# Optimization experiments

Measured on AMD Instinct MI355X. Metric: run time of the kernel, lower is better.

## Reference

```python
import jax, jax.numpy as jnp
import numpy as np

B, S, D, H = 4, 2048, 512, 8

def setup_inputs() -> dict:
    key = jax.random.key(0)
    ks = jax.random.split(key, 6)
    query = jax.random.normal(ks[0], (B, S, D), dtype=jnp.float32)
    value = jax.random.normal(ks[1], (B, S, D), dtype=jnp.float32)
    # causal additive mask, broadcast over heads: [H, S, S]
    causal = jnp.where(jnp.tril(jnp.ones((S, S), dtype=bool)), 0.0, -1e9).astype(jnp.float32)
    mask = jnp.broadcast_to(causal[None, :, :], (H, S, S))
    sd = 1.0 / np.sqrt(D)
    Wq = jax.random.normal(ks[2], (D, D), dtype=jnp.float32) * sd
    Wkv = jax.random.normal(ks[3], (D, 2 * D), dtype=jnp.float32) * sd
    Wo = jax.random.normal(ks[4], (D, D), dtype=jnp.float32) * sd
    normalizer = jnp.asarray(1.0 / np.sqrt(D // H), dtype=jnp.float32)  # 1/sqrt(head_size)
    head_mults = jnp.ones((1, 1, H, 1), dtype=jnp.float32)
    return {"query": query, "value": value, "mask": mask, "Wq": Wq, "Wkv": Wkv,
            "Wo": Wo, "normalizer": normalizer, "head_mults": head_mults}

def reference(query, value, mask, Wq, Wkv, Wo, normalizer, head_mults):
    b, sq, d = query.shape
    h = head_mults.shape[2]
    q = (query @ Wq).reshape(b, sq, h, -1)                 # [b,q,h,hd]
    k, v = jnp.split(value @ Wkv, 2, axis=-1)
    sk = value.shape[1]
    k = k.reshape(b, sk, h, -1)
    v = v.reshape(b, sk, h, -1)
    score = jnp.einsum('bqhd,bkhd->bhqk', q, k) * normalizer
    score = score + mask[None, :, :, :]
    align = jax.nn.softmax(score, axis=-1)
    heads = jnp.einsum('bhqk,bkhd->bqhd', align, v)        # [b,q,h,hd]
    # cross-head normalization (over head axis, ddof=0 like tf.reduce_std)
    mean = jnp.mean(heads, axis=-2, keepdims=True)
    std = jnp.std(heads, axis=-2, keepdims=True)
    heads = (heads - mean) / (std + 0.01)
    heads = heads * head_mults
    out = heads.reshape(b, sq, d) @ Wo
    return out
```

## Files before the change

### kernel.cpp

```cpp
#include <hip/hip_runtime.h>


typedef float  f32x4  __attribute__((ext_vector_type(4)));
typedef __bf16 bf16x8 __attribute__((ext_vector_type(8)));
typedef short  s16x4  __attribute__((ext_vector_type(4)));
typedef unsigned short u16;

#define BS 2048
#define DD 512
#define NH 8

__device__ __forceinline__ u16 f2bf(float f) {
  union { float f; unsigned u; } v; v.f = f;
  unsigned r = v.u + 0x7fffu + ((v.u >> 16) & 1u);
  return (u16)(r >> 16);
}
__device__ __forceinline__ float bf2f(u16 b) {
  union { unsigned u; float f; } v; v.u = ((unsigned)b) << 16; return v.f;
}
__device__ __forceinline__ u16 cvt1(float f) {
  __bf16 h = (__bf16)f;
  return __builtin_bit_cast(u16, h);
}

__device__ __forceinline__ void gll16(const u16* g, u16* l) {
  __builtin_amdgcn_global_load_lds((const __attribute__((address_space(1))) void*)g,
                                   (__attribute__((address_space(3))) void*)l, 16, 0, 0);
}

__global__ __launch_bounds__(256) void prep(const float* __restrict__ Wq,
                                            const float* __restrict__ Wkv,
                                            const float* __restrict__ Wo,
                                            u16* __restrict__ WqT, u16* __restrict__ WkvT,
                                            u16* __restrict__ WoT) {
  __shared__ float Ts[64][65];
  const int t = threadIdx.x;
  int tb = blockIdx.x;
  const float* W; u16* Wt; int N, ntn;
  if (tb < 64)       { W = Wq;  Wt = WqT;  N = 512;  ntn = 8; }
  else if (tb < 192) { W = Wkv; Wt = WkvT; N = 1024; ntn = 16; tb -= 64; }
  else               { W = Wo;  Wt = WoT;  N = 512;  ntn = 8;  tb -= 192; }
  int tk = tb / ntn, tn = tb - tk * ntn;
  int r = t >> 2, c0 = (t & 3) * 16;
  const float* src = &W[(long)(tk * 64 + r) * N + tn * 64 + c0];
#pragma unroll
  for (int j = 0; j < 4; ++j) {
    float4 x = *(const float4*)(src + j * 4);
    Ts[r][c0 + j * 4 + 0] = x.x; Ts[r][c0 + j * 4 + 1] = x.y;
    Ts[r][c0 + j * 4 + 2] = x.z; Ts[r][c0 + j * 4 + 3] = x.w;
  }
  __syncthreads();
  u16* dst = &Wt[(long)(tn * 64 + r) * 512 + tk * 64 + c0];
#pragma unroll
  for (int m = 0; m < 4; ++m) {
    ushort4 o;
    o.x = f2bf(Ts[c0 + m * 4 + 0][r]); o.y = f2bf(Ts[c0 + m * 4 + 1][r]);
    o.z = f2bf(Ts[c0 + m * 4 + 2][r]); o.w = f2bf(Ts[c0 + m * 4 + 3][r]);
    *(ushort4*)(dst + m * 4) = o;
  }
}

template <int AF32>
__device__ __forceinline__ void gemm_core64(const void* __restrict__ Av,
                                            const u16* __restrict__ Bt,
                                            int m0, int n0, int K,
                                            u16* Al, u16* Bl, f32x4 acc[4][4]) {
  const int t = threadIdx.x;
  const int wv = t >> 6, ln = t & 63, qd = ln >> 4, l16 = ln & 15;
  const int rw = (wv & 1) * 64, cw = (wv >> 1) * 64;
  const int srB = wv * 16 + (ln >> 2), scB = (ln & 3) * 8;
  const int srA = t >> 1, scA = (t & 1) * 16;
  for (int k0 = 0; k0 < K; k0 += 64) {
    __syncthreads();
    if (AF32) {
      const float* Af = (const float*)Av;
#pragma unroll
      for (int p = 0; p < 2; ++p) {
        const float* src = &Af[(long)(m0 + srA) * K + k0 + p * 32 + scA];
        float4 x0 = *(const float4*)src;
        float4 x1 = *(const float4*)(src + 4);
        float4 x2 = *(const float4*)(src + 8);
        float4 x3 = *(const float4*)(src + 12);
        bf16x8 o0, o1;
        o0[0] = (__bf16)x0.x; o0[1] = (__bf16)x0.y; o0[2] = (__bf16)x0.z; o0[3] = (__bf16)x0.w;
        o0[4] = (__bf16)x1.x; o0[5] = (__bf16)x1.y; o0[6] = (__bf16)x1.z; o0[7] = (__bf16)x1.w;
        o1[0] = (__bf16)x2.x; o1[1] = (__bf16)x2.y; o1[2] = (__bf16)x2.z; o1[3] = (__bf16)x2.w;
        o1[4] = (__bf16)x3.x; o1[5] = (__bf16)x3.y; o1[6] = (__bf16)x3.z; o1[7] = (__bf16)x3.w;
        u16* dst = &Al[p * 4096 + srA * 32 + scA];
        *(bf16x8*)dst = o0;
        *(bf16x8*)(dst + 8) = o1;
      }
    } else {
      const u16* Ab = (const u16*)Av;
#pragma unroll
      for (int p = 0; p < 2; ++p)
#pragma unroll
        for (int c = 0; c < 2; ++c) {
          int r = c * 64 + srB;
          gll16(&Ab[(long)(m0 + r) * K + k0 + p * 32 + scB], &Al[p * 4096 + r * 32 + scB]);
        }
    }
#pragma unroll
    for (int p = 0; p < 2; ++p)
#pragma unroll
      for (int c = 0; c < 2; ++c) {
        int r = c * 64 + srB;
        gll16(&Bt[(long)(n0 + r) * K + k0 + p * 32 + scB], &Bl[p * 4096 + r * 32 + scB]);
      }
    __syncthreads();
#pragma unroll
    for (int p = 0; p < 2; ++p) {
      bf16x8 af[4], bfr[4];
#pragma unroll
      for (int i = 0; i < 4; ++i)
        af[i] = *(const bf16x8*)&Al[p * 4096 + (rw + i * 16 + l16) * 32 + qd * 8];
#pragma unroll
      for (int j = 0; j < 4; ++j)
        bfr[j] = *(const bf16x8*)&Bl[p * 4096 + (cw + j * 16 + l16) * 32 + qd * 8];
#pragma unroll
      for (int i = 0; i < 4; ++i)
#pragma unroll
        for (int j = 0; j < 4; ++j)
          acc[i][j] = __builtin_amdgcn_mfma_f32_16x16x32_bf16(af[i], bfr[j], acc[i][j], 0, 0, 0);
    }
  }
}

__global__ __launch_bounds__(256) void qkv_gemm(const float* __restrict__ query,
                                                const float* __restrict__ value,
                                                const u16* __restrict__ WqT,
                                                const u16* __restrict__ WkvT,
                                                u16* __restrict__ Qb,
                                                u16* __restrict__ Kb,
                                                u16* __restrict__ Vt) {
  __shared__ __align__(16) u16 Al[2 * 128 * 32];
  __shared__ __align__(16) u16 Bl[2 * 128 * 32];
  const bool isQ = blockIdx.y < 4;
  const void* A = isQ ? (const void*)query : (const void*)value;
  const u16* Bt = isQ ? WqT : WkvT;
  const int n0 = (isQ ? blockIdx.y : blockIdx.y - 4) * 128;
  const int m0 = blockIdx.x * 128;
  f32x4 acc[4][4] = {};
  gemm_core64<1>(A, Bt, m0, n0, 512, Al, Bl, acc);
  const int t = threadIdx.x;
  const int wv = t >> 6, ln = t & 63, qd = ln >> 4, l16 = ln & 15;
  const int rw = (wv & 1) * 64, cw = (wv >> 1) * 64;
  if (isQ) {
#pragma unroll
    for (int i = 0; i < 4; ++i)
#pragma unroll
      for (int j = 0; j < 4; ++j) {
        int row = m0 + rw + i * 16 + qd * 4, col = n0 + cw + j * 16 + l16;
#pragma unroll
        for (int r = 0; r < 4; ++r)
          Qb[(long)(row + r) * 512 + col] = cvt1(acc[i][j][r]);
      }
  } else {
#pragma unroll
    for (int j = 0; j < 4; ++j) {
      int col = n0 + cw + j * 16 + l16;
      if (col < 512) {
#pragma unroll
        for (int i = 0; i < 4; ++i) {
          int row = m0 + rw + i * 16 + qd * 4;
#pragma unroll
          for (int r = 0; r < 4; ++r)
            Kb[(long)(row + r) * 512 + col] = cvt1(acc[i][j][r]);
        }
      } else {
        int c2 = col - 512, hh = c2 >> 6, dd = c2 & 63;
#pragma unroll
        for (int i = 0; i < 4; ++i) {
          int sg = m0 + rw + i * 16 + qd * 4;
          int bb = sg >> 11, ss = sg & 2047;
          ushort4 o;
          o.x = cvt1(acc[i][j][0]); o.y = cvt1(acc[i][j][1]);
          o.z = cvt1(acc[i][j][2]); o.w = cvt1(acc[i][j][3]);
          *(ushort4*)&Vt[((long)(bb * 8 + hh) * 64 + dd) * 2048 + ss] = o;
        }
      }
    }
  }
}

__global__ __launch_bounds__(256) void out_gemm(const u16* __restrict__ A,
                                                const u16* __restrict__ Bt,
                                                float* __restrict__ C) {
  __shared__ __align__(16) u16 Al[2 * 128 * 32];
  __shared__ __align__(16) u16 Bl[2 * 128 * 32];
  const int m0 = blockIdx.x * 128, n0 = blockIdx.y * 128;
  f32x4 acc[4][4] = {};
  gemm_core64<0>(A, Bt, m0, n0, 512, Al, Bl, acc);
  const int t = threadIdx.x;
  const int wv = t >> 6, ln = t & 63, qd = ln >> 4, l16 = ln & 15;
  const int rw = (wv & 1) * 64, cw = (wv >> 1) * 64;
#pragma unroll
  for (int i = 0; i < 4; ++i)
#pragma unroll
    for (int j = 0; j < 4; ++j) {
      int row = m0 + rw + i * 16 + qd * 4, col = n0 + cw + j * 16 + l16;
#pragma unroll
      for (int r = 0; r < 4; ++r)
        C[(long)(row + r) * 512 + col] = acc[i][j][r];
    }
}

__device__ __forceinline__ void attn_phase(const u16* ks, const u16* vs,
                                           const bf16x8 bq[2], f32x4 o[4],
                                           float& l_i, float scale2, bool diag,
                                           int wv, int qd, int l16) {
  constexpr int ST = 72;
  f32x4 s[4] = {};
#pragma unroll
  for (int c = 0; c < 2; ++c)
#pragma unroll
    for (int nt = 0; nt < 4; ++nt) {
      bf16x8 ak = *(const bf16x8*)&ks[(nt * 16 + l16) * ST + c * 32 + qd * 8];
      s[nt] = __builtin_amdgcn_mfma_f32_16x16x32_bf16(ak, bq[c], s[nt], 0, 0, 0);
    }
  if (diag) {
    const int limi = wv * 16 + l16;
#pragma unroll
    for (int nt = 0; nt < 4; ++nt)
#pragma unroll
      for (int r = 0; r < 4; ++r) {
        float v = s[nt][r] * scale2;
        if (nt * 16 + qd * 4 + r > limi) v = -INFINITY;
        float p = exp2f(v);
        s[nt][r] = p;
        l_i += p;
      }
  } else {
#pragma unroll
    for (int nt = 0; nt < 4; ++nt)
#pragma unroll
      for (int r = 0; r < 4; ++r) {
        float p = exp2f(s[nt][r] * scale2);
        s[nt][r] = p;
        l_i += p;
      }
  }
#pragma unroll
  for (int cp = 0; cp < 2; ++cp) {
    bf16x8 pb;
#pragma unroll
    for (int j = 0; j < 4; ++j) {
      pb[j] = (__bf16)s[cp * 2][j];
      pb[4 + j] = (__bf16)s[cp * 2 + 1][j];
    }
#pragma unroll
    for (int n2 = 0; n2 < 4; ++n2) {
      bf16x8 av;
      s16x4* ah = (s16x4*)&av;
      const u16* vp = &vs[(n2 * 16 + l16) * ST + cp * 32 + qd * 4];
      ah[0] = *(const s16x4*)vp;
      ah[1] = *(const s16x4*)(vp + 16);
      o[n2] = __builtin_amdgcn_mfma_f32_16x16x32_bf16(av, pb, o[n2], 0, 0, 0);
    }
  }
}

__global__ __launch_bounds__(256, 2) void attn(const u16* __restrict__ Qb,
                                               const u16* __restrict__ Kb,
                                               const u16* __restrict__ Vt,
                                               u16* __restrict__ heads,
                                               const float* __restrict__ normp) {
  constexpr int ST = 72;
  __shared__ __align__(16) u16 Ks[2][64 * ST];
  __shared__ __align__(16) u16 Vts[2][64 * ST];
  const float scale2 = normp[0] * 1.44269504f;
  const int t = threadIdx.x;
  const int wv = t >> 6, ln = t & 63, qd = ln >> 4, l16 = ln & 15;
  const int sr = t >> 2, scg = (t & 3) * 16;
  const int bid = blockIdx.x;
  const int hb = (bid & 7) + 8 * (bid >> 7);
  const int qtS = (bid >> 3) & 15, qtL = 31 - qtS;
  const int h = hb & 7, b = hb >> 3;
  const int bs0 = b * BS;
  const u16* vtb = Vt + ((long)(b * 8 + h) * 64) * 2048;

  bf16x8 bqS[2], bqL[2];
#pragma unroll
  for (int c = 0; c < 2; ++c) {
    bqS[c] = *(const bf16x8*)&Qb[(long)(bs0 + qtS * 64 + wv * 16 + l16) * 512 + h * 64 + c * 32 + qd * 8];
    bqL[c] = *(const bf16x8*)&Qb[(long)(bs0 + qtL * 64 + wv * 16 + l16) * 512 + h * 64 + c * 32 + qd * 8];
  }

  bf16x8 kr0, kr1, vr0, vr1;
#define FETCH(KB) do { \
    const u16* kp_ = &Kb[(long)(bs0 + (KB) * 64 + sr) * 512 + h * 64 + scg]; \
    kr0 = *(const bf16x8*)kp_; kr1 = *(const bf16x8*)(kp_ + 8); \
    const u16* vp_ = &vtb[(long)sr * 2048 + (KB) * 64 + scg]; \
    vr0 = *(const bf16x8*)vp_; vr1 = *(const bf16x8*)(vp_ + 8); } while (0)
  FETCH(0);
  float lS = 0.f, lL = 0.f;
  f32x4 oS[4] = {}, oL[4] = {};

  for (int kb = 0; kb <= qtL; ++kb) {
    const int buf = kb & 1;
    *(bf16x8*)&Ks[buf][sr * ST + scg] = kr0;
    *(bf16x8*)&Ks[buf][sr * ST + scg + 8] = kr1;
    *(bf16x8*)&Vts[buf][sr * ST + scg] = vr0;
    *(bf16x8*)&Vts[buf][sr * ST + scg + 8] = vr1;
    __syncthreads();
    if (kb < qtL) FETCH(kb + 1);

    attn_phase(Ks[buf], Vts[buf], bqL, oL, lL, scale2, kb == qtL, wv, qd, l16);
    if (kb <= qtS)
      attn_phase(Ks[buf], Vts[buf], bqS, oS, lS, scale2, kb == qtS, wv, qd, l16);
  }
#undef FETCH

  lL += __shfl_xor(lL, 16); lL += __shfl_xor(lL, 32);
  lS += __shfl_xor(lS, 16); lS += __shfl_xor(lS, 32);
  float invL = 1.f / lL, invS = 1.f / lS;
  __syncthreads();
#pragma unroll
  for (int n2 = 0; n2 < 4; ++n2)
#pragma unroll
    for (int r = 0; r < 4; ++r) {
      Ks[0][(wv * 16 + l16) * ST + n2 * 16 + qd * 4 + r] = cvt1(oL[n2][r] * invL);
      Vts[0][(wv * 16 + l16) * ST + n2 * 16 + qd * 4 + r] = cvt1(oS[n2][r] * invS);
    }
  __syncthreads();
  {
    u16* dstL = &heads[(long)(bs0 + qtL * 64 + sr) * 512 + h * 64 + scg];
    *(bf16x8*)dstL = *(const bf16x8*)&Ks[0][sr * ST + scg];
    *(bf16x8*)(dstL + 8) = *(const bf16x8*)&Ks[0][sr * ST + scg + 8];
    u16* dstS = &heads[(long)(bs0 + qtS * 64 + sr) * 512 + h * 64 + scg];
    *(bf16x8*)dstS = *(const bf16x8*)&Vts[0][sr * ST + scg];
    *(bf16x8*)(dstS + 8) = *(const bf16x8*)&Vts[0][sr * ST + scg + 8];
  }
}

__global__ __launch_bounds__(256) void headnorm(const u16* __restrict__ heads,
                                                const float* __restrict__ hm,
                                                u16* __restrict__ outn) {
  int i = blockIdx.x * 256 + threadIdx.x;
  int d = i & 63, bs = i >> 6;
  const u16* p = heads + (long)bs * DD + d;
  float x[NH], mean = 0.f;
#pragma unroll
  for (int h = 0; h < NH; ++h) { x[h] = bf2f(p[h * 64]); mean += x[h]; }
  mean *= 0.125f;
  float var = 0.f;
#pragma unroll
  for (int h = 0; h < NH; ++h) { float dd = x[h] - mean; var += dd * dd; }
  var *= 0.125f;
  float inv = 1.f / (sqrtf(var) + 0.01f);
#pragma unroll
  for (int h = 0; h < NH; ++h)
    outn[(long)bs * DD + h * 64 + d] = cvt1((x[h] - mean) * inv * hm[h]);
}

extern "C" void kernel_launch(void* const* d_in, const int* in_sizes, int n_in,
                              void* d_out, int out_size, void* d_ws, size_t ws_size,
                              hipStream_t stream) {
  const float* query = (const float*)d_in[0];
  const float* value = (const float*)d_in[1];
  const float* Wq    = (const float*)d_in[3];
  const float* Wkv   = (const float*)d_in[4];
  const float* Wo    = (const float*)d_in[5];
  const float* normp = (const float*)d_in[6];
  const float* hmult = (const float*)d_in[7];

  char* ws = (char*)d_ws;
  const size_t MB = 1 << 20;
  u16*   WqT   = (u16*)(ws);
  u16*   WkvT  = (u16*)(ws + 524288);
  u16*   WoT   = (u16*)(ws + 1 * MB + 524288);
  u16*   Qb    = (u16*)(ws + 2 * MB);
  u16*   Kb    = (u16*)(ws + 10 * MB);
  u16*   Vt    = (u16*)(ws + 18 * MB);
  u16*   heads = (u16*)(ws + 26 * MB);
  u16*   hN    = (u16*)(ws + 34 * MB);

  prep<<<256, 256, 0, stream>>>(Wq, Wkv, Wo, WqT, WkvT, WoT);
  qkv_gemm<<<dim3(64, 12), 256, 0, stream>>>(query, value, WqT, WkvT, Qb, Kb, Vt);
  attn<<<512, 256, 0, stream>>>(Qb, Kb, Vt, heads, normp);
  headnorm<<<(4 * BS * 64) / 256, 256, 0, stream>>>(heads, hmult, hN);
  out_gemm<<<dim3(64, 4), 256, 0, stream>>>(hN, WoT, (float*)d_out);
}
```

Before: 281.3 us.

## Fuse all five stages into one cooperative persistent kernel with grid syncs

```diff
diff --git a/kernel.cpp b/kernel.cpp
--- a/kernel.cpp
+++ b/kernel.cpp
@@ -1,5 +1,8 @@
 #include <hip/hip_runtime.h>
-
+#include <hip/hip_cooperative_groups.h>
+
+
+namespace cg = cooperative_groups;
 
 typedef float  f32x4  __attribute__((ext_vector_type(4)));
 typedef __bf16 bf16x8 __attribute__((ext_vector_type(8)));
@@ -28,14 +31,13 @@
                                    (__attribute__((address_space(3))) void*)l, 16, 0, 0);
 }
 
-__global__ __launch_bounds__(256) void prep(const float* __restrict__ Wq,
-                                            const float* __restrict__ Wkv,
-                                            const float* __restrict__ Wo,
-                                            u16* __restrict__ WqT, u16* __restrict__ WkvT,
-                                            u16* __restrict__ WoT) {
-  __shared__ float Ts[64][65];
-  const int t = threadIdx.x;
-  int tb = blockIdx.x;
+
+__device__ __forceinline__ void prep_body(int tb, int t,
+                                          const float* __restrict__ Wq,
+                                          const float* __restrict__ Wkv,
+                                          const float* __restrict__ Wo,
+                                          u16* __restrict__ WqT, u16* __restrict__ WkvT,
+                                          u16* __restrict__ WoT, float (*Ts)[65]) {
   const float* W; u16* Wt; int N, ntn;
   if (tb < 64)       { W = Wq;  Wt = WqT;  N = 512;  ntn = 8; }
   else if (tb < 192) { W = Wkv; Wt = WkvT; N = 1024; ntn = 16; tb -= 64; }
@@ -126,6 +128,289 @@
   }
 }
 
+__device__ __forceinline__ void qkv_tile(int bx, int by,
+                                         const float* __restrict__ query,
+                                         const float* __restrict__ value,
+                                         const u16* __restrict__ WqT,
+                                         const u16* __restrict__ WkvT,
+                                         u16* __restrict__ Qb, u16* __restrict__ Kb,
+                                         u16* __restrict__ Vt, u16* Al, u16* Bl) {
+  const bool isQ = by < 4;
+  const void* A = isQ ? (const void*)query : (const void*)value;
+  const u16* Bt = isQ ? WqT : WkvT;
+  const int n0 = (isQ ? by : by - 4) * 128;
+  const int m0 = bx * 128;
+  f32x4 acc[4][4] = {};
+  gemm_core64<1>(A, Bt, m0, n0, 512, Al, Bl, acc);
+  const int t = threadIdx.x;
+  const int wv = t >> 6, ln = t & 63, qd = ln >> 4, l16 = ln & 15;
+  const int rw = (wv & 1) * 64, cw = (wv >> 1) * 64;
+  if (isQ) {
+#pragma unroll
+    for (int i = 0; i < 4; ++i)
+#pragma unroll
+      for (int j = 0; j < 4; ++j) {
+        int row = m0 + rw + i * 16 + qd * 4, col = n0 + cw + j * 16 + l16;
+#pragma unroll
+        for (int r = 0; r < 4; ++r)
+          Qb[(long)(row + r) * 512 + col] = cvt1(acc[i][j][r]);
+      }
+  } else {
+#pragma unroll
+    for (int j = 0; j < 4; ++j) {
+      int col = n0 + cw + j * 16 + l16;
+      if (col < 512) {
+#pragma unroll
+        for (int i = 0; i < 4; ++i) {
+          int row = m0 + rw + i * 16 + qd * 4;
+#pragma unroll
+          for (int r = 0; r < 4; ++r)
+            Kb[(long)(row + r) * 512 + col] = cvt1(acc[i][j][r]);
+        }
+      } else {
+        int c2 = col - 512, hh = c2 >> 6, dd = c2 & 63;
+#pragma unroll
+        for (int i = 0; i < 4; ++i) {
+          int sg = m0 + rw + i * 16 + qd * 4;
+          int bb = sg >> 11, ss = sg & 2047;
+          ushort4 o;
+          o.x = cvt1(acc[i][j][0]); o.y = cvt1(acc[i][j][1]);
+          o.z = cvt1(acc[i][j][2]); o.w = cvt1(acc[i][j][3]);
+          *(ushort4*)&Vt[((long)(bb * 8 + hh) * 64 + dd) * 2048 + ss] = o;
+        }
+      }
+    }
+  }
+}
+
+__device__ __forceinline__ void out_tile(int bx, int by,
+                                         const u16* __restrict__ A,
+                                         const u16* __restrict__ Bt,
+                                         float* __restrict__ C, u16* Al, u16* Bl) {
+  const int m0 = bx * 128, n0 = by * 128;
+  f32x4 acc[4][4] = {};
+  gemm_core64<0>(A, Bt, m0, n0, 512, Al, Bl, acc);
+  const int t = threadIdx.x;
+  const int wv = t >> 6, ln = t & 63, qd = ln >> 4, l16 = ln & 15;
+  const int rw = (wv & 1) * 64, cw = (wv >> 1) * 64;
+#pragma unroll
+  for (int i = 0; i < 4; ++i)
+#pragma unroll
+    for (int j = 0; j < 4; ++j) {
+      int row = m0 + rw + i * 16 + qd * 4, col = n0 + cw + j * 16 + l16;
+#pragma unroll
+      for (int r = 0; r < 4; ++r)
+        C[(long)(row + r) * 512 + col] = acc[i][j][r];
+    }
+}
+
+__device__ __forceinline__ void attn_phase(const u16* ks, const u16* vs,
+                                           const bf16x8 bq[2], f32x4 o[4],
+                                           float& l_i, float scale2, bool diag,
+                                           int wv, int qd, int l16) {
+  constexpr int ST = 72;
+  f32x4 s[4] = {};
+#pragma unroll
+  for (int c = 0; c < 2; ++c)
+#pragma unroll
+    for (int nt = 0; nt < 4; ++nt) {
+      bf16x8 ak = *(const bf16x8*)&ks[(nt * 16 + l16) * ST + c * 32 + qd * 8];
+      s[nt] = __builtin_amdgcn_mfma_f32_16x16x32_bf16(ak, bq[c], s[nt], 0, 0, 0);
+    }
+  if (diag) {
+    const int limi = wv * 16 + l16;
+#pragma unroll
+    for (int nt = 0; nt < 4; ++nt)
+#pragma unroll
+      for (int r = 0; r < 4; ++r) {
+        float v = s[nt][r] * scale2;
+        if (nt * 16 + qd * 4 + r > limi) v = -INFINITY;
+        float p = exp2f(v);
+        s[nt][r] = p;
+        l_i += p;
+      }
+  } else {
+#pragma unroll
+    for (int nt = 0; nt < 4; ++nt)
+#pragma unroll
+      for (int r = 0; r < 4; ++r) {
+        float p = exp2f(s[nt][r] * scale2);
+        s[nt][r] = p;
+        l_i += p;
+      }
+  }
+#pragma unroll
+  for (int cp = 0; cp < 2; ++cp) {
+    bf16x8 pb;
+#pragma unroll
+    for (int j = 0; j < 4; ++j) {
+      pb[j] = (__bf16)s[cp * 2][j];
+      pb[4 + j] = (__bf16)s[cp * 2 + 1][j];
+    }
+#pragma unroll
+    for (int n2 = 0; n2 < 4; ++n2) {
+      bf16x8 av;
+      s16x4* ah = (s16x4*)&av;
+      const u16* vp = &vs[(n2 * 16 + l16) * ST + cp * 32 + qd * 4];
+      ah[0] = *(const s16x4*)vp;
+      ah[1] = *(const s16x4*)(vp + 16);
+      o[n2] = __builtin_amdgcn_mfma_f32_16x16x32_bf16(av, pb, o[n2], 0, 0, 0);
+    }
+  }
+}
+
+__device__ __forceinline__ void attn_block(int bid,
+                                           const u16* __restrict__ Qb,
+                                           const u16* __restrict__ Kb,
+                                           const u16* __restrict__ Vt,
+                                           u16* __restrict__ heads, float scale2,
+                                           u16* KsB, u16* VtsB) {
+  constexpr int ST = 72;
+  constexpr int BUF = 64 * ST;
+  const int t = threadIdx.x;
+  const int wv = t >> 6, ln = t & 63, qd = ln >> 4, l16 = ln & 15;
+  const int sr = t >> 2, scg = (t & 3) * 16;
+  const int hb = (bid & 7) + 8 * (bid >> 7);
+  const int qtS = (bid >> 3) & 15, qtL = 31 - qtS;
+  const int h = hb & 7, b = hb >> 3;
+  const int bs0 = b * BS;
+  const u16* vtb = Vt + ((long)(b * 8 + h) * 64) * 2048;
+
+  bf16x8 bqS[2], bqL[2];
+#pragma unroll
+  for (int c = 0; c < 2; ++c) {
+    bqS[c] = *(const bf16x8*)&Qb[(long)(bs0 + qtS * 64 + wv * 16 + l16) * 512 + h * 64 + c * 32 + qd * 8];
+    bqL[c] = *(const bf16x8*)&Qb[(long)(bs0 + qtL * 64 + wv * 16 + l16) * 512 + h * 64 + c * 32 + qd * 8];
+  }
+
+  bf16x8 kr0, kr1, vr0, vr1;
+#define FETCH(KB) do { \
+    const u16* kp_ = &Kb[(long)(bs0 + (KB) * 64 + sr) * 512 + h * 64 + scg]; \
+    kr0 = *(const bf16x8*)kp_; kr1 = *(const bf16x8*)(kp_ + 8); \
+    const u16* vp_ = &vtb[(long)sr * 2048 + (KB) * 64 + scg]; \
+    vr0 = *(const bf16x8*)vp_; vr1 = *(const bf16x8*)(vp_ + 8); } while (0)
+  FETCH(0);
+  float lS = 0.f, lL = 0.f;
+  f32x4 oS[4] = {}, oL[4] = {};
+
+  for (int kb = 0; kb <= qtL; ++kb) {
+    u16* Ksb = KsB + (kb & 1) * BUF;
+    u16* Vtsb = VtsB + (kb & 1) * BUF;
+    *(bf16x8*)&Ksb[sr * ST + scg] = kr0;
+    *(bf16x8*)&Ksb[sr * ST + scg + 8] = kr1;
+    *(bf16x8*)&Vtsb[sr * ST + scg] = vr0;
+    *(bf16x8*)&Vtsb[sr * ST + scg + 8] = vr1;
+    __syncthreads();
+    if (kb < qtL) FETCH(kb + 1);
+
+    attn_phase(Ksb, Vtsb, bqL, oL, lL, scale2, kb == qtL, wv, qd, l16);
+    if (kb <= qtS)
+      attn_phase(Ksb, Vtsb, bqS, oS, lS, scale2, kb == qtS, wv, qd, l16);
+  }
+#undef FETCH
+
+  lL += __shfl_xor(lL, 16); lL += __shfl_xor(lL, 32);
+  lS += __shfl_xor(lS, 16); lS += __shfl_xor(lS, 32);
+  float invL = 1.f / lL, invS = 1.f / lS;
+  __syncthreads();
+#pragma unroll
+  for (int n2 = 0; n2 < 4; ++n2)
+#pragma unroll
+    for (int r = 0; r < 4; ++r) {
+      KsB[(wv * 16 + l16) * ST + n2 * 16 + qd * 4 + r] = cvt1(oL[n2][r] * invL);
+      VtsB[(wv * 16 + l16) * ST + n2 * 16 + qd * 4 + r] = cvt1(oS[n2][r] * invS);
+    }
+  __syncthreads();
+  {
+    u16* dstL = &heads[(long)(bs0 + qtL * 64 + sr) * 512 + h * 64 + scg];
+    *(bf16x8*)dstL = *(const bf16x8*)&KsB[sr * ST + scg];
+    *(bf16x8*)(dstL + 8) = *(const bf16x8*)&KsB[sr * ST + scg + 8];
+    u16* dstS = &heads[(long)(bs0 + qtS * 64 + sr) * 512 + h * 64 + scg];
+    *(bf16x8*)dstS = *(const bf16x8*)&VtsB[sr * ST + scg];
+    *(bf16x8*)(dstS + 8) = *(const bf16x8*)&VtsB[sr * ST + scg + 8];
+  }
+}
+
+__device__ __forceinline__ void headnorm_i(int i, const u16* __restrict__ heads,
+                                           const float* __restrict__ hm,
+                                           u16* __restrict__ outn) {
+  int d = i & 63, bs = i >> 6;
+  const u16* p = heads + (long)bs * DD + d;
+  float x[NH], mean = 0.f;
+#pragma unroll
+  for (int h = 0; h < NH; ++h) { x[h] = bf2f(p[h * 64]); mean += x[h]; }
+  mean *= 0.125f;
+  float var = 0.f;
+#pragma unroll
+  for (int h = 0; h < NH; ++h) { float dd = x[h] - mean; var += dd * dd; }
+  var *= 0.125f;
+  float inv = 1.f / (sqrtf(var) + 0.01f);
+#pragma unroll
+  for (int h = 0; h < NH; ++h)
+    outn[(long)bs * DD + h * 64 + d] = cvt1((x[h] - mean) * inv * hm[h]);
+}
+
+__global__ __launch_bounds__(256, 2) void fused(const float* __restrict__ query,
+                                                const float* __restrict__ value,
+                                                const float* __restrict__ Wq,
+                                                const float* __restrict__ Wkv,
+                                                const float* __restrict__ Wo,
+                                                const float* __restrict__ normp,
+                                                const float* __restrict__ hmult,
+                                                u16* __restrict__ WqT,
+                                                u16* __restrict__ WkvT,
+                                                u16* __restrict__ WoT,
+                                                u16* __restrict__ Qb,
+                                                u16* __restrict__ Kb,
+                                                u16* __restrict__ Vt,
+                                                u16* __restrict__ heads,
+                                                u16* __restrict__ hN,
+                                                float* __restrict__ out) {
+  __shared__ __align__(16) unsigned char smraw[36864];
+  const int t = threadIdx.x;
+  const int bid = blockIdx.x;
+  cg::grid_group grid = cg::this_grid();
+  const float scale2 = normp[0] * 1.44269504f;
+
+  if (bid < 256)
+    prep_body(bid, t, Wq, Wkv, Wo, WqT, WkvT, WoT, (float(*)[65])smraw);
+  __threadfence();
+  grid.sync();
+
+  {
+    u16* Al = (u16*)smraw;
+    u16* Bl = (u16*)(smraw + 16384);
+    for (int tile = bid; tile < 768; tile += 512)
+      qkv_tile(tile & 63, tile >> 6, query, value, WqT, WkvT, Qb, Kb, Vt, Al, Bl);
+  }
+  __threadfence();
+  grid.sync();
+
+  attn_block(bid, Qb, Kb, Vt, heads, scale2, (u16*)smraw, (u16*)(smraw + 18432));
+  __threadfence();
+  grid.sync();
+
+  for (int i = bid * 256 + t; i < 4 * BS * 64; i += 512 * 256)
+    headnorm_i(i, heads, hmult, hN);
+  __threadfence();
+  grid.sync();
+
+  if (bid < 256) {
+    u16* Al = (u16*)smraw;
+    u16* Bl = (u16*)(smraw + 16384);
+    out_tile(bid & 63, bid >> 6, hN, WoT, out, Al, Bl);
+  }
+}
+
+__global__ __launch_bounds__(256) void prep(const float* __restrict__ Wq,
+                                            const float* __restrict__ Wkv,
+                                            const float* __restrict__ Wo,
+                                            u16* __restrict__ WqT, u16* __restrict__ WkvT,
+                                            u16* __restrict__ WoT) {
+  __shared__ float Ts[64][65];
+  prep_body(blockIdx.x, threadIdx.x, Wq, Wkv, Wo, WqT, WkvT, WoT, Ts);
+}
+
 __global__ __launch_bounds__(256) void qkv_gemm(const float* __restrict__ query,
                                                 const float* __restrict__ value,
                                                 const u16* __restrict__ WqT,
@@ -135,52 +420,23 @@
                                                 u16* __restrict__ Vt) {
   __shared__ __align__(16) u16 Al[2 * 128 * 32];
   __shared__ __align__(16) u16 Bl[2 * 128 * 32];
-  const bool isQ = blockIdx.y < 4;
-  const void* A = isQ ? (const void*)query : (const void*)value;
-  const u16* Bt = isQ ? WqT : WkvT;
-  const int n0 = (isQ ? blockIdx.y : blockIdx.y - 4) * 128;
-  const int m0 = blockIdx.x * 128;
-  f32x4 acc[4][4] = {};
-  gemm_core64<1>(A, Bt, m0, n0, 512, Al, Bl, acc);
-  const int t = threadIdx.x;
-  const int wv = t >> 6, ln = t & 63, qd = ln >> 4, l16 = ln & 15;
-  const int rw = (wv & 1) * 64, cw = (wv >> 1) * 64;
-  if (isQ) {
-#pragma unroll
-    for (int i = 0; i < 4; ++i)
-#pragma unroll
-      for (int j = 0; j < 4; ++j) {
-        int row = m0 + rw + i * 16 + qd * 4, col = n0 + cw + j * 16 + l16;
-#pragma unroll
-        for (int r = 0; r < 4; ++r)
-          Qb[(long)(row + r) * 512 + col] = cvt1(acc[i][j][r]);
-      }
-  } else {
-#pragma unroll
-    for (int j = 0; j < 4; ++j) {
-      int col = n0 + cw + j * 16 + l16;
-      if (col < 512) {
-#pragma unroll
-        for (int i = 0; i < 4; ++i) {
-          int row = m0 + rw + i * 16 + qd * 4;
-#pragma unroll
-          for (int r = 0; r < 4; ++r)
-            Kb[(long)(row + r) * 512 + col] = cvt1(acc[i][j][r]);
-        }
-      } else {
-        int c2 = col - 512, hh = c2 >> 6, dd = c2 & 63;
-#pragma unroll
-        for (int i = 0; i < 4; ++i) {
-          int sg = m0 + rw + i * 16 + qd * 4;
-          int bb = sg >> 11, ss = sg & 2047;
-          ushort4 o;
-          o.x = cvt1(acc[i][j][0]); o.y = cvt1(acc[i][j][1]);
-          o.z = cvt1(acc[i][j][2]); o.w = cvt1(acc[i][j][3]);
-          *(ushort4*)&Vt[((long)(bb * 8 + hh) * 64 + dd) * 2048 + ss] = o;
-        }
-      }
-    }
-  }
+  qkv_tile(blockIdx.x, blockIdx.y, query, value, WqT, WkvT, Qb, Kb, Vt, Al, Bl);
+}
+
+__global__ __launch_bounds__(256, 2) void attn(const u16* __restrict__ Qb,
+                                               const u16* __restrict__ Kb,
+                                               const u16* __restrict__ Vt,
+                                               u16* __restrict__ heads,
+                                               const float* __restrict__ normp) {
+  __shared__ __align__(16) u16 KsB[2 * 64 * 72];
+  __shared__ __align__(16) u16 VtsB[2 * 64 * 72];
+  attn_block(blockIdx.x, Qb, Kb, Vt, heads, normp[0] * 1.44269504f, KsB, VtsB);
+}
+
+__global__ __launch_bounds__(256) void headnorm(const u16* __restrict__ heads,
+                                                const float* __restrict__ hm,
+                                                u16* __restrict__ outn) {
+  headnorm_i(blockIdx.x * 256 + threadIdx.x, heads, hm, outn);
 }
 
 __global__ __launch_bounds__(256) void out_gemm(const u16* __restrict__ A,
@@ -188,169 +444,7 @@
                                                 float* __restrict__ C) {
   __shared__ __align__(16) u16 Al[2 * 128 * 32];
   __shared__ __align__(16) u16 Bl[2 * 128 * 32];
-  const int m0 = blockIdx.x * 128, n0 = blockIdx.y * 128;
-  f32x4 acc[4][4] = {};
-  gemm_core64<0>(A, Bt, m0, n0, 512, Al, Bl, acc);
-  const int t = threadIdx.x;
-  const int wv = t >> 6, ln = t & 63, qd = ln >> 4, l16 = ln & 15;
-  const int rw = (wv & 1) * 64, cw = (wv >> 1) * 64;
-#pragma unroll
-  for (int i = 0; i < 4; ++i)
-#pragma unroll
-    for (int j = 0; j < 4; ++j) {
-      int row = m0 + rw + i * 16 + qd * 4, col = n0 + cw + j * 16 + l16;
-#pragma unroll
-      for (int r = 0; r < 4; ++r)
-        C[(long)(row + r) * 512 + col] = acc[i][j][r];
-    }
-}
-
-__device__ __forceinline__ void attn_phase(const u16* ks, const u16* vs,
-                                           const bf16x8 bq[2], f32x4 o[4],
-                                           float& l_i, float scale2, bool diag,
-                                           int wv, int qd, int l16) {
-  constexpr int ST = 72;
-  f32x4 s[4] = {};
-#pragma unroll
-  for (int c = 0; c < 2; ++c)
-#pragma unroll
-    for (int nt = 0; nt < 4; ++nt) {
-      bf16x8 ak = *(const bf16x8*)&ks[(nt * 16 + l16) * ST + c * 32 + qd * 8];
-      s[nt] = __builtin_amdgcn_mfma_f32_16x16x32_bf16(ak, bq[c], s[nt], 0, 0, 0);
-    }
-  if (diag) {
-    const int limi = wv * 16 + l16;
-#pragma unroll
-    for (int nt = 0; nt < 4; ++nt)
-#pragma unroll
-      for (int r = 0; r < 4; ++r) {
-        float v = s[nt][r] * scale2;
-        if (nt * 16 + qd * 4 + r > limi) v = -INFINITY;
-        float p = exp2f(v);
-        s[nt][r] = p;
-        l_i += p;
-      }
-  } else {
-#pragma unroll
-    for (int nt = 0; nt < 4; ++nt)
-#pragma unroll
-      for (int r = 0; r < 4; ++r) {
-        float p = exp2f(s[nt][r] * scale2);
-        s[nt][r] = p;
-        l_i += p;
-      }
-  }
-#pragma unroll
-  for (int cp = 0; cp < 2; ++cp) {
-    bf16x8 pb;
-#pragma unroll
-    for (int j = 0; j < 4; ++j) {
-      pb[j] = (__bf16)s[cp * 2][j];
-      pb[4 + j] = (__bf16)s[cp * 2 + 1][j];
-    }
-#pragma unroll
-    for (int n2 = 0; n2 < 4; ++n2) {
-      bf16x8 av;
-      s16x4* ah = (s16x4*)&av;
-      const u16* vp = &vs[(n2 * 16 + l16) * ST + cp * 32 + qd * 4];
-      ah[0] = *(const s16x4*)vp;
-      ah[1] = *(const s16x4*)(vp + 16);
-      o[n2] = __builtin_amdgcn_mfma_f32_16x16x32_bf16(av, pb, o[n2], 0, 0, 0);
-    }
-  }
-}
-
-__global__ __launch_bounds__(256, 2) void attn(const u16* __restrict__ Qb,
-                                               const u16* __restrict__ Kb,
-                                               const u16* __restrict__ Vt,
-                                               u16* __restrict__ heads,
-                                               const float* __restrict__ normp) {
-  constexpr int ST = 72;
-  __shared__ __align__(16) u16 Ks[2][64 * ST];
-  __shared__ __align__(16) u16 Vts[2][64 * ST];
-  const float scale2 = normp[0] * 1.44269504f;
-  const int t = threadIdx.x;
-  const int wv = t >> 6, ln = t & 63, qd = ln >> 4, l16 = ln & 15;
-  const int sr = t >> 2, scg = (t & 3) * 16;
-  const int bid = blockIdx.x;
-  const int hb = (bid & 7) + 8 * (bid >> 7);
-  const int qtS = (bid >> 3) & 15, qtL = 31 - qtS;
-  const int h = hb & 7, b = hb >> 3;
-  const int bs0 = b * BS;
-  const u16* vtb = Vt + ((long)(b * 8 + h) * 64) * 2048;
-
-  bf16x8 bqS[2], bqL[2];
-#pragma unroll
-  for (int c = 0; c < 2; ++c) {
-    bqS[c] = *(const bf16x8*)&Qb[(long)(bs0 + qtS * 64 + wv * 16 + l16) * 512 + h * 64 + c * 32 + qd * 8];
-    bqL[c] = *(const bf16x8*)&Qb[(long)(bs0 + qtL * 64 + wv * 16 + l16) * 512 + h * 64 + c * 32 + qd * 8];
-  }
-
-  bf16x8 kr0, kr1, vr0, vr1;
-#define FETCH(KB) do { \
-    const u16* kp_ = &Kb[(long)(bs0 + (KB) * 64 + sr) * 512 + h * 64 + scg]; \
-    kr0 = *(const bf16x8*)kp_; kr1 = *(const bf16x8*)(kp_ + 8); \
-    const u16* vp_ = &vtb[(long)sr * 2048 + (KB) * 64 + scg]; \
-    vr0 = *(const bf16x8*)vp_; vr1 = *(const bf16x8*)(vp_ + 8); } while (0)
-  FETCH(0);
-  float lS = 0.f, lL = 0.f;
-  f32x4 oS[4] = {}, oL[4] = {};
-
-  for (int kb = 0; kb <= qtL; ++kb) {
-    const int buf = kb & 1;
-    *(bf16x8*)&Ks[buf][sr * ST + scg] = kr0;
-    *(bf16x8*)&Ks[buf][sr * ST + scg + 8] = kr1;
-    *(bf16x8*)&Vts[buf][sr * ST + scg] = vr0;
-    *(bf16x8*)&Vts[buf][sr * ST + scg + 8] = vr1;
-    __syncthreads();
-    if (kb < qtL) FETCH(kb + 1);
-
-    attn_phase(Ks[buf], Vts[buf], bqL, oL, lL, scale2, kb == qtL, wv, qd, l16);
-    if (kb <= qtS)
-      attn_phase(Ks[buf], Vts[buf], bqS, oS, lS, scale2, kb == qtS, wv, qd, l16);
-  }
-#undef FETCH
-
-  lL += __shfl_xor(lL, 16); lL += __shfl_xor(lL, 32);
-  lS += __shfl_xor(lS, 16); lS += __shfl_xor(lS, 32);
-  float invL = 1.f / lL, invS = 1.f / lS;
-  __syncthreads();
-#pragma unroll
-  for (int n2 = 0; n2 < 4; ++n2)
-#pragma unroll
-    for (int r = 0; r < 4; ++r) {
-      Ks[0][(wv * 16 + l16) * ST + n2 * 16 + qd * 4 + r] = cvt1(oL[n2][r] * invL);
-      Vts[0][(wv * 16 + l16) * ST + n2 * 16 + qd * 4 + r] = cvt1(oS[n2][r] * invS);
-    }
-  __syncthreads();
-  {
-    u16* dstL = &heads[(long)(bs0 + qtL * 64 + sr) * 512 + h * 64 + scg];
-    *(bf16x8*)dstL = *(const bf16x8*)&Ks[0][sr * ST + scg];
-    *(bf16x8*)(dstL + 8) = *(const bf16x8*)&Ks[0][sr * ST + scg + 8];
-    u16* dstS = &heads[(long)(bs0 + qtS * 64 + sr) * 512 + h * 64 + scg];
-    *(bf16x8*)dstS = *(const bf16x8*)&Vts[0][sr * ST + scg];
-    *(bf16x8*)(dstS + 8) = *(const bf16x8*)&Vts[0][sr * ST + scg + 8];
-  }
-}
-
-__global__ __launch_bounds__(256) void headnorm(const u16* __restrict__ heads,
-                                                const float* __restrict__ hm,
-                                                u16* __restrict__ outn) {
-  int i = blockIdx.x * 256 + threadIdx.x;
-  int d = i & 63, bs = i >> 6;
-  const u16* p = heads + (long)bs * DD + d;
-  float x[NH], mean = 0.f;
-#pragma unroll
-  for (int h = 0; h < NH; ++h) { x[h] = bf2f(p[h * 64]); mean += x[h]; }
-  mean *= 0.125f;
-  float var = 0.f;
-#pragma unroll
-  for (int h = 0; h < NH; ++h) { float dd = x[h] - mean; var += dd * dd; }
-  var *= 0.125f;
-  float inv = 1.f / (sqrtf(var) + 0.01f);
-#pragma unroll
-  for (int h = 0; h < NH; ++h)
-    outn[(long)bs * DD + h * 64 + d] = cvt1((x[h] - mean) * inv * hm[h]);
+  out_tile(blockIdx.x, blockIdx.y, A, Bt, C, Al, Bl);
 }
 
 extern "C" void kernel_launch(void* const* d_in, const int* in_sizes, int n_in,
@@ -374,10 +468,19 @@
   u16*   Vt    = (u16*)(ws + 18 * MB);
   u16*   heads = (u16*)(ws + 26 * MB);
   u16*   hN    = (u16*)(ws + 34 * MB);
-
-  prep<<<256, 256, 0, stream>>>(Wq, Wkv, Wo, WqT, WkvT, WoT);
-  qkv_gemm<<<dim3(64, 12), 256, 0, stream>>>(query, value, WqT, WkvT, Qb, Kb, Vt);
-  attn<<<512, 256, 0, stream>>>(Qb, Kb, Vt, heads, normp);
-  headnorm<<<(4 * BS * 64) / 256, 256, 0, stream>>>(heads, hmult, hN);
-  out_gemm<<<dim3(64, 4), 256, 0, stream>>>(hN, WoT, (float*)d_out);
-}
+  float* outf  = (float*)d_out;
+
+  void* args[] = {(void*)&query, (void*)&value, (void*)&Wq, (void*)&Wkv, (void*)&Wo,
+                  (void*)&normp, (void*)&hmult, (void*)&WqT, (void*)&WkvT, (void*)&WoT,
+                  (void*)&Qb, (void*)&Kb, (void*)&Vt, (void*)&heads, (void*)&hN,
+                  (void*)&outf};
+  hipError_t err = hipLaunchCooperativeKernel((const void*)fused, dim3(512), dim3(256),
+                                              args, 0, stream);
+  if (err != hipSuccess) {
+    prep<<<256, 256, 0, stream>>>(Wq, Wkv, Wo, WqT, WkvT, WoT);
+    qkv_gemm<<<dim3(64, 12), 256, 0, stream>>>(query, value, WqT, WkvT, Qb, Kb, Vt);
+    attn<<<512, 256, 0, stream>>>(Qb, Kb, Vt, heads, normp);
+    headnorm<<<(4 * BS * 64) / 256, 256, 0, stream>>>(heads, hmult, hN);
+    out_gemm<<<dim3(64, 4), 256, 0, stream>>>(hN, WoT, outf);
+  }
+}
```

Result: slower. 758.4 us (+169.6%).

## Process two K/V tiles per barrier with quad-buffered shared memory

Applied to the files above, without the earlier changes.

```diff
diff --git a/kernel.cpp b/kernel.cpp
--- a/kernel.cpp
+++ b/kernel.cpp
@@ -266,8 +266,9 @@
                                                u16* __restrict__ heads,
                                                const float* __restrict__ normp) {
   constexpr int ST = 72;
-  __shared__ __align__(16) u16 Ks[2][64 * ST];
-  __shared__ __align__(16) u16 Vts[2][64 * ST];
+  constexpr int BUF = 64 * ST;
+  __shared__ __align__(16) u16 Ks[4][BUF];
+  __shared__ __align__(16) u16 Vts[4][BUF];
   const float scale2 = normp[0] * 1.44269504f;
   const int t = threadIdx.x;
   const int wv = t >> 6, ln = t & 63, qd = ln >> 4, l16 = ln & 15;
@@ -278,6 +279,7 @@
   const int h = hb & 7, b = hb >> 3;
   const int bs0 = b * BS;
   const u16* vtb = Vt + ((long)(b * 8 + h) * 64) * 2048;
+  const int scL = qtL >> 1;
 
   bf16x8 bqS[2], bqL[2];
 #pragma unroll
@@ -286,28 +288,41 @@
     bqL[c] = *(const bf16x8*)&Qb[(long)(bs0 + qtL * 64 + wv * 16 + l16) * 512 + h * 64 + c * 32 + qd * 8];
   }
 
-  bf16x8 kr0, kr1, vr0, vr1;
-#define FETCH(KB) do { \
-    const u16* kp_ = &Kb[(long)(bs0 + (KB) * 64 + sr) * 512 + h * 64 + scg]; \
+  bf16x8 kr0, kr1, kr2, kr3, vr0, vr1, vr2, vr3;
+#define FETCH(SC) do { \
+    const u16* kp_ = &Kb[(long)(bs0 + (SC) * 128 + sr) * 512 + h * 64 + scg]; \
     kr0 = *(const bf16x8*)kp_; kr1 = *(const bf16x8*)(kp_ + 8); \
-    const u16* vp_ = &vtb[(long)sr * 2048 + (KB) * 64 + scg]; \
-    vr0 = *(const bf16x8*)vp_; vr1 = *(const bf16x8*)(vp_ + 8); } while (0)
+    const u16* kp2_ = kp_ + (long)64 * 512; \
+    kr2 = *(const bf16x8*)kp2_; kr3 = *(const bf16x8*)(kp2_ + 8); \
+    const u16* vp_ = &vtb[(long)sr * 2048 + (SC) * 128 + scg]; \
+    vr0 = *(const bf16x8*)vp_; vr1 = *(const bf16x8*)(vp_ + 8); \
+    vr2 = *(const bf16x8*)(vp_ + 64); vr3 = *(const bf16x8*)(vp_ + 72); } while (0)
   FETCH(0);
   float lS = 0.f, lL = 0.f;
   f32x4 oS[4] = {}, oL[4] = {};
 
-  for (int kb = 0; kb <= qtL; ++kb) {
-    const int buf = kb & 1;
-    *(bf16x8*)&Ks[buf][sr * ST + scg] = kr0;
-    *(bf16x8*)&Ks[buf][sr * ST + scg + 8] = kr1;
-    *(bf16x8*)&Vts[buf][sr * ST + scg] = vr0;
-    *(bf16x8*)&Vts[buf][sr * ST + scg + 8] = vr1;
+  for (int sc = 0; sc <= scL; ++sc) {
+    const int sub0 = 2 * sc, sub1 = 2 * sc + 1;
+    const int b0 = sub0 & 3, b1 = sub1 & 3;
+    *(bf16x8*)&Ks[b0][sr * ST + scg] = kr0;
+    *(bf16x8*)&Ks[b0][sr * ST + scg + 8] = kr1;
+    *(bf16x8*)&Ks[b1][sr * ST + scg] = kr2;
+    *(bf16x8*)&Ks[b1][sr * ST + scg + 8] = kr3;
+    *(bf16x8*)&Vts[b0][sr * ST + scg] = vr0;
+    *(bf16x8*)&Vts[b0][sr * ST + scg + 8] = vr1;
+    *(bf16x8*)&Vts[b1][sr * ST + scg] = vr2;
+    *(bf16x8*)&Vts[b1][sr * ST + scg + 8] = vr3;
     __syncthreads();
-    if (kb < qtL) FETCH(kb + 1);
-
-    attn_phase(Ks[buf], Vts[buf], bqL, oL, lL, scale2, kb == qtL, wv, qd, l16);
-    if (kb <= qtS)
-      attn_phase(Ks[buf], Vts[buf], bqS, oS, lS, scale2, kb == qtS, wv, qd, l16);
+    if (sc < scL) FETCH(sc + 1);
+
+    attn_phase(Ks[b0], Vts[b0], bqL, oL, lL, scale2, sub0 == qtL, wv, qd, l16);
+    if (sub0 <= qtS)
+      attn_phase(Ks[b0], Vts[b0], bqS, oS, lS, scale2, sub0 == qtS, wv, qd, l16);
+    if (sub1 <= qtL) {
+      attn_phase(Ks[b1], Vts[b1], bqL, oL, lL, scale2, sub1 == qtL, wv, qd, l16);
+      if (sub1 <= qtS)
+        attn_phase(Ks[b1], Vts[b1], bqS, oS, lS, scale2, sub1 == qtS, wv, qd, l16);
+    }
   }
 #undef FETCH
 
```

After: 281.9 us. About the same (+0.2%).
